# Performance work log

Hardware: AMD Instinct MI355X
Metric: run time of the kernel (lower is better)

The kernel has to match this reference:

```python
import jax, jax.numpy as jnp
import numpy as np

NEG_INF = -1e9

def setup_inputs() -> dict:
    key = jax.random.key(0)
    k1, k2, k3, k4, k5 = jax.random.split(key, 5)
    B, Lq, Lk, D = 8, 2048, 2048, 256
    query = jax.random.normal(k1, (B, Lq, D), dtype=jnp.float32)
    key_t = jax.random.normal(k2, (B, Lk, D), dtype=jnp.float32)
    value = jax.random.normal(k3, (B, Lk, D), dtype=jnp.float32)
    mask = jax.random.randint(k4, (B, Lq, Lk), 0, 2, dtype=jnp.int32)
    # nn.Linear(d_k, 1, bias=False) weight, flattened to [d_k]
    w_align = jax.random.normal(k5, (D,), dtype=jnp.float32) / jnp.sqrt(jnp.float32(D))
    return {"query": query, "key": key_t, "value": value, "mask": mask, "w_align": w_align}

def reference(query, key, value, mask, w_align):
    # Bahdanau additive scores: w . (q_i + k_j). Since the alignment layer is
    # linear, distribute it: score[b,i,j] = (q[b,i] . w) + (k[b,j] . w),
    # avoiding the [B,Lq,Lk,D] broadcast intermediate (same math exactly).
    sq = jnp.einsum('bqd,d->bq', query, w_align)   # [B,Lq]
    sk = jnp.einsum('bkd,d->bk', key, w_align)     # [B,Lk]
    scores = sq[:, :, None] + sk[:, None, :]       # [B,Lq,Lk]
    scores = jnp.where(mask == 0, NEG_INF, scores)
    p_attn = jax.nn.softmax(scores, axis=-1)
    return jnp.matmul(p_attn, value)               # [B,Lq,Dv]
```

## Files before the change

### kernel.cpp

```cpp
#include <hip/hip_runtime.h>
#include <hip/hip_bf16.h>


#define NB 8
#define LQ 2048
#define LK 2048
#define DD 256

typedef __attribute__((ext_vector_type(8))) short short8v;
typedef __attribute__((ext_vector_type(8))) unsigned short ushort8v;
typedef __attribute__((ext_vector_type(4))) float f32x4;

__device__ inline unsigned short f2bf(float x) {
  union { __hip_bfloat16 h; unsigned short u; } cv;
  cv.h = __float2bfloat16(x);
  return cv.u;
}

__device__ inline void gld_lds16(const unsigned short* g, unsigned short* l) {
  __builtin_amdgcn_global_load_lds(
      (const __attribute__((address_space(1))) void*)g,
      (__attribute__((address_space(3))) void*)l, 16, 0, 0);
}

__global__ __launch_bounds__(256) void bah_precompute(
    const float* __restrict__ key, const float* __restrict__ value,
    const float* __restrict__ w, unsigned short* __restrict__ evT,
    unsigned short* __restrict__ eb)
{
  __shared__ float w_s[DD];
  __shared__ unsigned short t_s[64][DD];

  const int t = threadIdx.x;
  const int lane = t & 63;
  const int wid = t >> 6;
  const int blk = blockIdx.x;
  const int b = blk & 7;
  const int j0 = (blk >> 3) * 64;

  w_s[t] = w[t];
  __syncthreads();
  const float4 wv4 = reinterpret_cast<const float4*>(w_s)[lane];

  for (int it = 0; it < 16; ++it) {
    const int r = it * 4 + wid;
    const size_t row = (size_t)b * LK + (j0 + r);
    const float4 kv = reinterpret_cast<const float4*>(key + row * DD)[lane];
    float s = kv.x * wv4.x + kv.y * wv4.y + kv.z * wv4.z + kv.w * wv4.w;
#pragma unroll
    for (int off = 32; off; off >>= 1) s += __shfl_xor(s, off);
    const float e = __expf(s);
    if (lane == 0) eb[row] = f2bf(e);
    const float4 vv = reinterpret_cast<const float4*>(value + row * DD)[lane];
    ushort4 u;
    u.x = f2bf(e * vv.x);
    u.y = f2bf(e * vv.y);
    u.z = f2bf(e * vv.z);
    u.w = f2bf(e * vv.w);
    *reinterpret_cast<ushort4*>(&t_s[r][lane * 4]) = u;
  }
  __syncthreads();

  const int d = t;
  unsigned short* dst = evT + ((size_t)b * DD + d) * LK + j0;
#pragma unroll
  for (int s8 = 0; s8 < 8; ++s8) {
    ushort8v val;
#pragma unroll
    for (int c = 0; c < 8; ++c) val[c] = t_s[s8 * 8 + c][d];
    *reinterpret_cast<ushort8v*>(dst + s8 * 8) = val;
  }
}

__global__ __launch_bounds__(512, 2) void bah_gemm(
    const int* __restrict__ mask, const unsigned short* __restrict__ evT,
    const unsigned short* __restrict__ eb, float* __restrict__ out)
{
  __shared__ unsigned short A_s[2][64 * 64];
  __shared__ unsigned short B_s[2][DD * 64];
  __shared__ unsigned short e_s[LK];
  __shared__ float denom_s[64];

  const int t = threadIdx.x;
  const int lane = t & 63;
  const int wid = t >> 6;
  const int wm = wid >> 2;
  const int wn = wid & 3;
  const int lr = lane & 15;
  const int lk = (lane >> 4) * 8;

  const int blk = blockIdx.x;
  const int b = blk & 7;
  const int i0 = (blk >> 3) * 64;

  const int sr = t >> 3;
  const int sc = (t & 7) * 8;
  const int sslot = (((t & 7) ^ (sr & 7)) * 8);
  const int* mrow = mask + ((size_t)b * LQ + (i0 + sr)) * LK;

  const unsigned short* evTb = evT + (size_t)b * DD * LK;
  const int bswz = ((lane & 7) ^ (lane >> 3)) * 8;
  const int brow0 = wid * 32;
  const int brl = lane >> 3;

  *reinterpret_cast<ushort4*>(&e_s[t * 4]) =
      *reinterpret_cast<const ushort4*>(eb + (size_t)b * LK + t * 4);

  {
    const int4 a0 = *reinterpret_cast<const int4*>(mrow + sc);
    const int4 a1 = *reinterpret_cast<const int4*>(mrow + sc + 4);
#pragma unroll
    for (int s = 0; s < 4; ++s)
      gld_lds16(evTb + (size_t)(brow0 + s * 8 + brl) * LK + bswz,
                &B_s[0][(brow0 + s * 8) * 64]);
    ushort8v au;
    au[0] = a0.x ? 0x3F80 : 0;  au[1] = a0.y ? 0x3F80 : 0;
    au[2] = a0.z ? 0x3F80 : 0;  au[3] = a0.w ? 0x3F80 : 0;
    au[4] = a1.x ? 0x3F80 : 0;  au[5] = a1.y ? 0x3F80 : 0;
    au[6] = a1.z ? 0x3F80 : 0;  au[7] = a1.w ? 0x3F80 : 0;
    *reinterpret_cast<ushort8v*>(&A_s[0][sr * 64 + sslot]) = au;
  }
  __syncthreads();

  f32x4 acc[2][4] = {};
  f32x4 accd[2] = {};
  int buf = 0;

  for (int t32 = 0; t32 < 32; ++t32) {
    const int k0 = t32 * 64;
    const int kn = (t32 == 31) ? 0 : k0 + 64;

    const int4 a0 = *reinterpret_cast<const int4*>(mrow + kn + sc);
    const int4 a1 = *reinterpret_cast<const int4*>(mrow + kn + sc + 4);
    unsigned short* Bd = &B_s[buf ^ 1][0];
#pragma unroll
    for (int s = 0; s < 4; ++s)
      gld_lds16(evTb + (size_t)(brow0 + s * 8 + brl) * LK + kn + bswz,
                Bd + (brow0 + s * 8) * 64);

    const unsigned short* As = &A_s[buf][0];
    const unsigned short* Bs = &B_s[buf][0];
#pragma unroll
    for (int kk = 0; kk < 64; kk += 32) {
      const int kr = kk + lk;
      short8v af[2], bfv[4];
#pragma unroll
      for (int m = 0; m < 2; ++m) {
        const int row = wm * 32 + m * 16 + lr;
        af[m] = *reinterpret_cast<const short8v*>(&As[row * 64 + (kr ^ ((row & 7) * 8))]);
      }
#pragma unroll
      for (int n = 0; n < 4; ++n) {
        const int d = wn * 64 + n * 16 + lr;
        bfv[n] = *reinterpret_cast<const short8v*>(&Bs[d * 64 + (kr ^ ((d & 7) * 8))]);
      }
      if (wn == 0) {
        const short8v z8 = {};
        short8v ev = *reinterpret_cast<const short8v*>(&e_s[k0 + kr]);
        ev = (lr == 0) ? ev : z8;
#pragma unroll
        for (int m = 0; m < 2; ++m)
          accd[m] = __builtin_amdgcn_mfma_f32_16x16x32_bf16(af[m], ev, accd[m], 0, 0, 0);
      }
#pragma unroll
      for (int m = 0; m < 2; ++m)
#pragma unroll
        for (int n = 0; n < 4; ++n)
          acc[m][n] = __builtin_amdgcn_mfma_f32_16x16x32_bf16(af[m], bfv[n], acc[m][n], 0, 0, 0);
    }

    ushort8v au;
    au[0] = a0.x ? 0x3F80 : 0;  au[1] = a0.y ? 0x3F80 : 0;
    au[2] = a0.z ? 0x3F80 : 0;  au[3] = a0.w ? 0x3F80 : 0;
    au[4] = a1.x ? 0x3F80 : 0;  au[5] = a1.y ? 0x3F80 : 0;
    au[6] = a1.z ? 0x3F80 : 0;  au[7] = a1.w ? 0x3F80 : 0;
    *reinterpret_cast<ushort8v*>(&A_s[buf ^ 1][sr * 64 + sslot]) = au;

    __syncthreads();
    buf ^= 1;
  }

  if (wn == 0 && lr == 0) {
#pragma unroll
    for (int m = 0; m < 2; ++m)
#pragma unroll
      for (int r = 0; r < 4; ++r)
        denom_s[wm * 32 + m * 16 + (lane >> 4) * 4 + r] = accd[m][r];
  }
  __syncthreads();

#pragma unroll
  for (int m = 0; m < 2; ++m) {
    const int row0 = wm * 32 + m * 16 + ((lane >> 4) << 2);
    float inv[4];
#pragma unroll
    for (int r = 0; r < 4; ++r) {
      const float dn = denom_s[row0 + r];
      inv[r] = (dn != 0.f) ? 1.f / dn : 0.f;
    }
#pragma unroll
    for (int n = 0; n < 4; ++n) {
      const int col = wn * 64 + n * 16 + lr;
#pragma unroll
      for (int r = 0; r < 4; ++r)
        out[((size_t)b * LQ + (i0 + row0 + r)) * DD + col] = acc[m][n][r] * inv[r];
    }
  }
}

extern "C" void kernel_launch(void* const* d_in, const int* in_sizes, int n_in,
                              void* d_out, int out_size, void* d_ws, size_t ws_size,
                              hipStream_t stream) {
  const float* key   = (const float*)d_in[1];
  const float* value = (const float*)d_in[2];
  const int*   mask  = (const int*)d_in[3];
  const float* w     = (const float*)d_in[4];
  float* out = (float*)d_out;

  unsigned short* evT = (unsigned short*)d_ws;
  unsigned short* eb  = (unsigned short*)((char*)d_ws + (size_t)NB * DD * LK * 2);

  bah_precompute<<<NB * (LK / 64), 256, 0, stream>>>(key, value, w, evT, eb);
  bah_gemm<<<NB * (LQ / 64), 512, 0, stream>>>(mask, evT, eb, out);
}
```

Before: 62.41 us.

## Shrink GEMM tile to 32 rows and use triple-buffered K pipeline

```diff
diff --git a/kernel.cpp b/kernel.cpp
--- a/kernel.cpp
+++ b/kernel.cpp
@@ -6,6 +6,7 @@
 #define LQ 2048
 #define LK 2048
 #define DD 256
+#define BK 32
 
 typedef __attribute__((ext_vector_type(8))) short short8v;
 typedef __attribute__((ext_vector_type(8))) unsigned short ushort8v;
@@ -72,14 +73,14 @@
   }
 }
 
-__global__ __launch_bounds__(512, 2) void bah_gemm(
+__global__ __launch_bounds__(512, 4) void bah_gemm(
     const int* __restrict__ mask, const unsigned short* __restrict__ evT,
     const unsigned short* __restrict__ eb, float* __restrict__ out)
 {
-  __shared__ unsigned short A_s[2][64 * 64];
-  __shared__ unsigned short B_s[2][DD * 64];
+  __shared__ unsigned short A_s[3][32 * BK];
+  __shared__ unsigned short B_s[3][DD * BK];
   __shared__ unsigned short e_s[LK];
-  __shared__ float denom_s[64];
+  __shared__ float denom_s[32];
 
   const int t = threadIdx.x;
   const int lane = t & 63;
@@ -87,124 +88,116 @@
   const int wm = wid >> 2;
   const int wn = wid & 3;
   const int lr = lane & 15;
-  const int lk = (lane >> 4) * 8;
+  const int kq = lane >> 4;
 
   const int blk = blockIdx.x;
   const int b = blk & 7;
-  const int i0 = (blk >> 3) * 64;
-
-  const int sr = t >> 3;
-  const int sc = (t & 7) * 8;
-  const int sslot = (((t & 7) ^ (sr & 7)) * 8);
-  const int* mrow = mask + ((size_t)b * LQ + (i0 + sr)) * LK;
+  const int i0 = (blk >> 3) * 32;
+
+  const int ar = t >> 4;
+  const int ac = (t & 15) * 2;
+  const int aslot = ar * BK + (((ac >> 3) ^ ((ar >> 1) & 3)) * 8) + (ac & 7);
+  const int* aptr = mask + ((size_t)b * LQ + i0 + ar) * LK + ac;
 
   const unsigned short* evTb = evT + (size_t)b * DD * LK;
-  const int bswz = ((lane & 7) ^ (lane >> 3)) * 8;
-  const int brow0 = wid * 32;
-  const int brl = lane >> 3;
+  const int brow_in = lane >> 2;
+  const int bsrc_off = ((lane & 3) ^ ((lane >> 3) & 3)) * 8;
 
   *reinterpret_cast<ushort4*>(&e_s[t * 4]) =
       *reinterpret_cast<const ushort4*>(eb + (size_t)b * LK + t * 4);
 
+  const int arow = wm * 16 + lr;
+  const int aoff = arow * BK + ((kq ^ ((arow >> 1) & 3)) * 8);
+  int boff[4];
+#pragma unroll
+  for (int n = 0; n < 4; ++n) {
+    const int d = wn * 64 + n * 16 + lr;
+    boff[n] = d * BK + ((kq ^ ((d >> 1) & 3)) * 8);
+  }
+
   {
-    const int4 a0 = *reinterpret_cast<const int4*>(mrow + sc);
-    const int4 a1 = *reinterpret_cast<const int4*>(mrow + sc + 4);
-#pragma unroll
-    for (int s = 0; s < 4; ++s)
-      gld_lds16(evTb + (size_t)(brow0 + s * 8 + brl) * LK + bswz,
-                &B_s[0][(brow0 + s * 8) * 64]);
-    ushort8v au;
-    au[0] = a0.x ? 0x3F80 : 0;  au[1] = a0.y ? 0x3F80 : 0;
-    au[2] = a0.z ? 0x3F80 : 0;  au[3] = a0.w ? 0x3F80 : 0;
-    au[4] = a1.x ? 0x3F80 : 0;  au[5] = a1.y ? 0x3F80 : 0;
-    au[6] = a1.z ? 0x3F80 : 0;  au[7] = a1.w ? 0x3F80 : 0;
-    *reinterpret_cast<ushort8v*>(&A_s[0][sr * 64 + sslot]) = au;
-  }
-  __syncthreads();
-
-  f32x4 acc[2][4] = {};
-  f32x4 accd[2] = {};
-  int buf = 0;
-
-  for (int t32 = 0; t32 < 32; ++t32) {
-    const int k0 = t32 * 64;
-    const int kn = (t32 == 31) ? 0 : k0 + 64;
-
-    const int4 a0 = *reinterpret_cast<const int4*>(mrow + kn + sc);
-    const int4 a1 = *reinterpret_cast<const int4*>(mrow + kn + sc + 4);
-    unsigned short* Bd = &B_s[buf ^ 1][0];
-#pragma unroll
-    for (int s = 0; s < 4; ++s)
-      gld_lds16(evTb + (size_t)(brow0 + s * 8 + brl) * LK + kn + bswz,
-                Bd + (brow0 + s * 8) * 64);
-
-    const unsigned short* As = &A_s[buf][0];
-    const unsigned short* Bs = &B_s[buf][0];
-#pragma unroll
-    for (int kk = 0; kk < 64; kk += 32) {
-      const int kr = kk + lk;
-      short8v af[2], bfv[4];
-#pragma unroll
-      for (int m = 0; m < 2; ++m) {
-        const int row = wm * 32 + m * 16 + lr;
-        af[m] = *reinterpret_cast<const short8v*>(&As[row * 64 + (kr ^ ((row & 7) * 8))]);
-      }
-#pragma unroll
-      for (int n = 0; n < 4; ++n) {
-        const int d = wn * 64 + n * 16 + lr;
-        bfv[n] = *reinterpret_cast<const short8v*>(&Bs[d * 64 + (kr ^ ((d & 7) * 8))]);
-      }
-      if (wn == 0) {
-        const short8v z8 = {};
-        short8v ev = *reinterpret_cast<const short8v*>(&e_s[k0 + kr]);
-        ev = (lr == 0) ? ev : z8;
-#pragma unroll
-        for (int m = 0; m < 2; ++m)
-          accd[m] = __builtin_amdgcn_mfma_f32_16x16x32_bf16(af[m], ev, accd[m], 0, 0, 0);
-      }
-#pragma unroll
-      for (int m = 0; m < 2; ++m)
-#pragma unroll
-        for (int n = 0; n < 4; ++n)
-          acc[m][n] = __builtin_amdgcn_mfma_f32_16x16x32_bf16(af[m], bfv[n], acc[m][n], 0, 0, 0);
+    const int2 a0 = *reinterpret_cast<const int2*>(aptr);
+#pragma unroll
+    for (int g = 0; g < 2; ++g)
+      gld_lds16(evTb + (size_t)(wid * 32 + g * 16 + brow_in) * LK + bsrc_off,
+                &B_s[0][(wid * 32 + g * 16) * BK]);
+    const unsigned int aw0 = (a0.x ? 0x3F80u : 0u) | ((a0.y ? 0x3F80u : 0u) << 16);
+    *reinterpret_cast<unsigned int*>(&A_s[0][aslot]) = aw0;
+  }
+  int2 aregs = *reinterpret_cast<const int2*>(aptr + BK);
+#pragma unroll
+  for (int g = 0; g < 2; ++g)
+    gld_lds16(evTb + (size_t)(wid * 32 + g * 16 + brow_in) * LK + BK + bsrc_off,
+              &B_s[1][(wid * 32 + g * 16) * BK]);
+  __syncthreads();
+
+  unsigned short *Ac = A_s[0], *An1 = A_s[1], *An2 = A_s[2];
+  unsigned short *Bc = B_s[0], *Bn1 = B_s[1], *Bn2 = B_s[2];
+
+  f32x4 acc[4] = {};
+  f32x4 accd = {};
+  const short8v z8 = {};
+
+#pragma unroll 1
+  for (int t32 = 0; t32 < 64; ++t32) {
+    const int k2 = ((t32 + 2) & 63) * BK;
+    const int2 anew = *reinterpret_cast<const int2*>(aptr + k2);
+#pragma unroll
+    for (int g = 0; g < 2; ++g)
+      gld_lds16(evTb + (size_t)(wid * 32 + g * 16 + brow_in) * LK + k2 + bsrc_off,
+                Bn2 + (wid * 32 + g * 16) * BK);
+    __builtin_amdgcn_sched_barrier(0);
+
+    const short8v af = *reinterpret_cast<const short8v*>(&Ac[aoff]);
+    if (wn == 0) {
+      short8v ev = *reinterpret_cast<const short8v*>(&e_s[t32 * BK + kq * 8]);
+      ev = (lr == 0) ? ev : z8;
+      accd = __builtin_amdgcn_mfma_f32_16x16x32_bf16(af, ev, accd, 0, 0, 0);
     }
-
-    ushort8v au;
-    au[0] = a0.x ? 0x3F80 : 0;  au[1] = a0.y ? 0x3F80 : 0;
-    au[2] = a0.z ? 0x3F80 : 0;  au[3] = a0.w ? 0x3F80 : 0;
-    au[4] = a1.x ? 0x3F80 : 0;  au[5] = a1.y ? 0x3F80 : 0;
-    au[6] = a1.z ? 0x3F80 : 0;  au[7] = a1.w ? 0x3F80 : 0;
-    *reinterpret_cast<ushort8v*>(&A_s[buf ^ 1][sr * 64 + sslot]) = au;
-
-    __syncthreads();
-    buf ^= 1;
+#pragma unroll
+    for (int n = 0; n < 4; ++n) {
+      const short8v bfv = *reinterpret_cast<const short8v*>(&Bc[boff[n]]);
+      acc[n] = __builtin_amdgcn_mfma_f32_16x16x32_bf16(af, bfv, acc[n], 0, 0, 0);
+    }
+
+    __builtin_amdgcn_sched_barrier(0);
+    asm volatile("s_waitcnt vmcnt(3)");
+    __builtin_amdgcn_sched_barrier(0);
+
+    const unsigned int aw = (aregs.x ? 0x3F80u : 0u) | ((aregs.y ? 0x3F80u : 0u) << 16);
+    *reinterpret_cast<unsigned int*>(&An1[aslot]) = aw;
+
+    asm volatile("s_waitcnt lgkmcnt(0)");
+    __builtin_amdgcn_sched_barrier(0);
+    __builtin_amdgcn_s_barrier();
+    __builtin_amdgcn_sched_barrier(0);
+
+    aregs = anew;
+    unsigned short* tp;
+    tp = Ac; Ac = An1; An1 = An2; An2 = tp;
+    tp = Bc; Bc = Bn1; Bn1 = Bn2; Bn2 = tp;
   }
 
   if (wn == 0 && lr == 0) {
 #pragma unroll
-    for (int m = 0; m < 2; ++m)
-#pragma unroll
-      for (int r = 0; r < 4; ++r)
-        denom_s[wm * 32 + m * 16 + (lane >> 4) * 4 + r] = accd[m][r];
-  }
-  __syncthreads();
-
-#pragma unroll
-  for (int m = 0; m < 2; ++m) {
-    const int row0 = wm * 32 + m * 16 + ((lane >> 4) << 2);
-    float inv[4];
-#pragma unroll
-    for (int r = 0; r < 4; ++r) {
-      const float dn = denom_s[row0 + r];
-      inv[r] = (dn != 0.f) ? 1.f / dn : 0.f;
-    }
-#pragma unroll
-    for (int n = 0; n < 4; ++n) {
-      const int col = wn * 64 + n * 16 + lr;
-#pragma unroll
-      for (int r = 0; r < 4; ++r)
-        out[((size_t)b * LQ + (i0 + row0 + r)) * DD + col] = acc[m][n][r] * inv[r];
-    }
+    for (int r = 0; r < 4; ++r)
+      denom_s[wm * 16 + (lane >> 4) * 4 + r] = accd[r];
+  }
+  __syncthreads();
+
+  const int row0 = wm * 16 + (lane >> 4) * 4;
+  float inv[4];
+#pragma unroll
+  for (int r = 0; r < 4; ++r) {
+    const float dn = denom_s[row0 + r];
+    inv[r] = (dn != 0.f) ? 1.f / dn : 0.f;
+  }
+#pragma unroll
+  for (int n = 0; n < 4; ++n) {
+    const int col = wn * 64 + n * 16 + lr;
+#pragma unroll
+    for (int r = 0; r < 4; ++r)
+      out[((size_t)b * LQ + (i0 + row0 + r)) * DD + col] = acc[n][r] * inv[r];
   }
 }
 
@@ -221,5 +214,5 @@
   unsigned short* eb  = (unsigned short*)((char*)d_ws + (size_t)NB * DD * LK * 2);
 
   bah_precompute<<<NB * (LK / 64), 256, 0, stream>>>(key, value, w, evT, eb);
-  bah_gemm<<<NB * (LQ / 64), 512, 0, stream>>>(mask, evT, eb, out);
-}
+  bah_gemm<<<NB * (LQ / 32), 512, 0, stream>>>(mask, evT, eb, out);
+}
```

After: 67.17 us. 1.08x slower.
